# Kernel optimization log

Measured on AMD Instinct MI355X. Metric: run time of the kernel, lower is better.

The kernel has to match this reference:

```python
import jax, jax.numpy as jnp
import numpy as np

V, E, H = 50000, 256, 256   # vocab, emb_dim, hid_dim
R, S, W = 64, 32, 64        # reviews, sentences/review, words/sentence
UF = 20                     # user feature dim


def _bigru_last(x, wih, whh, bih, bhh):
    """Bidirectional GRU over x [B,T,D]; returns sum of final hidden states of
    the two directions, shape [B,H]. Params stacked over direction axis 0."""
    Hh = whh.shape[-1]

    def onedir(xd, wi, wh, bi, bh):
        gx = jnp.einsum('btd,gd->btg', xd, wi) + bi  # [B,T,3H] input gates precomputed

        def step(h, gxt):
            gh = h @ wh.T + bh
            r = jax.nn.sigmoid(gxt[:, :Hh] + gh[:, :Hh])
            z = jax.nn.sigmoid(gxt[:, Hh:2 * Hh] + gh[:, Hh:2 * Hh])
            n = jnp.tanh(gxt[:, 2 * Hh:] + r * gh[:, 2 * Hh:])
            return (1.0 - z) * n + z * h, None

        h0 = jnp.zeros((xd.shape[0], Hh), xd.dtype)
        hT, _ = jax.lax.scan(step, h0, jnp.swapaxes(gx, 0, 1))
        return hT

    return (onedir(x, wih[0], whh[0], bih[0], bhh[0])
            + onedir(x[:, ::-1], wih[1], whh[1], bih[1], bhh[1]))


def setup_inputs() -> dict:
    key = jax.random.key(0)
    ks = iter(jax.random.split(key, 40))

    def wmat(shape, scale=0.05):
        return jax.random.normal(next(ks), shape, jnp.float32) * scale

    inp = {}
    inp['inputs'] = jax.random.randint(next(ks), (R, S, W), 0, V)
    inp['sent_lengths'] = jax.random.randint(next(ks), (R, S), 1, W)
    inp['sent_counts'] = jax.random.randint(next(ks), (R,), 1, S)
    inp['user_feats'] = jax.random.normal(next(ks), (R, UF), jnp.float32)
    inp['embed'] = wmat((V, E))
    for name, din in (('wg', E), ('sg', H), ('rg', H + UF)):
        inp[name + '_wih'] = wmat((2, 3 * H, din))
        inp[name + '_whh'] = wmat((2, 3 * H, H))
        inp[name + '_bih'] = jnp.zeros((2, 3 * H), jnp.float32)
        inp[name + '_bhh'] = jnp.zeros((2, 3 * H), jnp.float32)
    inp['rfc_w1'] = wmat((H // 2, H + UF)); inp['rfc_b1'] = jnp.zeros((H // 2,), jnp.float32)
    inp['rfc_w2'] = wmat((1, H // 2));      inp['rfc_b2'] = jnp.zeros((1,), jnp.float32)
    inp['pfc_w1'] = wmat((H // 2, H));      inp['pfc_b1'] = jnp.zeros((H // 2,), jnp.float32)
    inp['pfc_w2'] = wmat((9, H // 2));      inp['pfc_b2'] = jnp.zeros((9,), jnp.float32)
    inp['uf_w'] = jnp.ones((UF,), jnp.float32)  # user_feats_weights
    return inp


def reference(inputs, sent_lengths, sent_counts, user_feats, embed,
              wg_wih, wg_whh, wg_bih, wg_bhh,
              sg_wih, sg_whh, sg_bih, sg_bhh,
              rg_wih, rg_whh, rg_bih, rg_bhh,
              rfc_w1, rfc_b1, rfc_w2, rfc_b2,
              pfc_w1, pfc_b1, pfc_w2, pfc_b2, uf_w):
    Rr, Sr, Wr = inputs.shape
    emb = embed[inputs]  # [R,S,W,E]  (dropout = identity in eval mode)
    # word-level bi-GRU, all R*S sentences batched together
    sent = _bigru_last(emb.reshape(Rr * Sr, Wr, emb.shape[-1]),
                       wg_wih, wg_whh, wg_bih, wg_bhh).reshape(Rr, Sr, -1)
    # sentence-level bi-GRU, batch over reviews
    rev = _bigru_last(sent, sg_wih, sg_whh, sg_bih, sg_bhh)  # [R,H]
    # F.normalize(user_feats) * user_feats_weights
    nrm = jnp.maximum(jnp.linalg.norm(user_feats, axis=-1, keepdims=True), 1e-12)
    p_batch = jnp.concatenate([rev, (user_feats / nrm) * uf_w], axis=-1)  # [R,H+20]
    r_stars = (jax.nn.selu(p_batch @ rfc_w1.T + rfc_b1) @ rfc_w2.T + rfc_b2)[:, 0]  # [R]
    # review-level bi-GRU over the sequence of reviews (batch 1)
    doc = _bigru_last(p_batch[None], rg_wih, rg_whh, rg_bih, rg_bhh)[0]  # [H]
    p_stars = jax.nn.selu(doc @ pfc_w1.T + pfc_b1) @ pfc_w2.T + pfc_b2  # [9]
    return p_stars, r_stars
```

## Files before the change

kernel.cpp:

```cpp
#include <hip/hip_runtime.h>
#include <math.h>

#define R_ 64
#define S_ 32
#define W_ 64
#define H_ 256
#define UF_ 20
#define TC 4

typedef short bf16x8 __attribute__((ext_vector_type(8)));
typedef float f32x4  __attribute__((ext_vector_type(4)));

#define MFMA(a,b,c) __builtin_amdgcn_mfma_f32_16x16x32_bf16((a),(b),(c),0,0,0)

__device__ __forceinline__ float sigf(float x){ return 1.0f/(1.0f+__expf(-x)); }
__device__ __forceinline__ float tanhf_(float x){ float e=__expf(2.0f*x); return 1.0f-2.0f/(e+1.0f); }
__device__ __forceinline__ float seluf_(float x){
  const float sc=1.0507009873554805f, al=1.6732632423543772f;
  return x>0.0f ? sc*x : sc*al*(expf(x)-1.0f);
}
__device__ __forceinline__ short tobf(float f){
  unsigned u=__float_as_uint(f); u += 0x7fffu + ((u>>16)&1u); return (short)(u>>16);
}
__device__ __forceinline__ float bf2f(short s){
  return __uint_as_float(((unsigned)(unsigned short)s) << 16);
}
__device__ __forceinline__ unsigned pk2(float a, float b){
  return (unsigned)(unsigned short)tobf(a) | ((unsigned)(unsigned short)tobf(b) << 16);
}

__global__ void prep_word_w(const float* __restrict__ wih, const float* __restrict__ whh,
                            short* __restrict__ Bw)
{
  int idx = blockIdx.x*256 + threadIdx.x;
  int lane = idx & 63;
  int rest = idx >> 6;
  int f  = rest % 6;  rest /= 6;
  int kt = rest % 16; rest /= 16;
  int w  = rest % 8;
  int d  = rest / 8;
  int gate = f >> 1;
  int j = 32*w + (f&1)*16 + (lane&15);
  int row = gate*256 + j;
  const float* W = (kt < 8 ? wih : whh) + (size_t)d*768*256;
  int k = (kt&7)*32 + (lane>>4)*8;
  short* dst = Bw + ((((size_t)(d*8 + w)*16 + kt)*6 + f)*64 + lane)*8;
#pragma unroll
  for (int jj=0;jj<8;jj++) dst[jj] = tobf(W[(size_t)row*256 + k + jj]);
}

__global__ void prep_rnn_w(const float* __restrict__ whh, short* __restrict__ Bs)
{
  int idx = blockIdx.x*256 + threadIdx.x;
  int lane = idx & 63;
  int rest = idx >> 6;
  int f  = rest % 6; rest /= 6;
  int kt = rest % 8; rest /= 8;
  int w  = rest % 8;
  int d  = rest / 8;
  int j = 32*w + (f&1)*16 + (lane&15);
  int row = (f>>1)*256 + j;
  const float* W = whh + (size_t)d*768*256;
  int k = kt*32 + (lane>>4)*8;
  short* dst = Bs + ((((size_t)(d*8 + w)*8 + kt)*6 + f)*64 + lane)*8;
#pragma unroll
  for (int jj=0;jj<8;jj++) dst[jj] = tobf(W[(size_t)row*256 + k + jj]);
}

__global__ void prep_gemm_w(const float* __restrict__ Wsrc, short* __restrict__ Bg)
{
  int idx = blockIdx.x*256 + threadIdx.x;
  int lane = idx & 63;
  int rest = idx >> 6;
  int kt = rest % 8;
  int nt = rest / 8;
  int n = nt*16 + (lane&15);
  int k = kt*32 + (lane>>4)*8;
  short* dst = Bg + (((size_t)nt*8 + kt)*64 + lane)*8;
#pragma unroll
  for (int jj=0;jj<8;jj++) dst[jj] = tobf(Wsrc[(size_t)n*256 + k + jj]);
}

__global__ __launch_bounds__(256) void gemm_gxu(
    const short* __restrict__ Ab, const float* __restrict__ Af,
    const int* __restrict__ toks, const short* __restrict__ Bg,
    short* __restrict__ C, long Czoff,
    int mode, int t0, int Mclamp, int Cstride)
{
  const int z  = blockIdx.z;
  const int m0 = blockIdx.x * 64;
  const int yt = blockIdx.y * 8;
  const int ntb = (mode == 2 ? z*48 : 0) + yt;
  const int tid = threadIdx.x;
  const int w = tid >> 6, l = tid & 63;
  const int c = l & 15, q = l >> 4;
  __shared__ short As[64][264];
  {
    const int row = tid >> 2, c0 = (tid & 3) * 64;
    if (mode == 0) {
      const uint4* s = (const uint4*)(Ab + (size_t)(m0+row)*256 + c0);
#pragma unroll
      for (int i = 0; i < 8; i++) *(uint4*)&As[row][c0 + i*8] = s[i];
    } else {
      int r;
      if (mode == 1) {
        r = m0 + row; if (r >= Mclamp) r = Mclamp - 1;
      } else {
        const int rr = m0 + row;
        const int s_ = rr / TC, i_ = rr % TC;
        const int wd = z ? (63 - (t0 + i_)) : (t0 + i_);
        r = toks[s_*64 + wd];
      }
      const float* s = Af + (size_t)r*256 + c0;
#pragma unroll
      for (int i = 0; i < 8; i++) {
        float4 v0 = *(const float4*)(s + i*8);
        float4 v1 = *(const float4*)(s + i*8 + 4);
        uint4 u;
        u.x = pk2(v0.x, v0.y); u.y = pk2(v0.z, v0.w);
        u.z = pk2(v1.x, v1.y); u.w = pk2(v1.z, v1.w);
        *(uint4*)&As[row][c0 + i*8] = u;
      }
    }
  }
  __syncthreads();
  f32x4 acc[4][2];
#pragma unroll
  for (int a = 0; a < 4; a++) { acc[a][0] = (f32x4)0.f; acc[a][1] = (f32x4)0.f; }
#pragma unroll
  for (int kt = 0; kt < 8; kt++) {
    const int ko = kt*32 + q*8;
    bf16x8 a0 = *(const bf16x8*)&As[ 0+c][ko];
    bf16x8 a1 = *(const bf16x8*)&As[16+c][ko];
    bf16x8 a2 = *(const bf16x8*)&As[32+c][ko];
    bf16x8 a3 = *(const bf16x8*)&As[48+c][ko];
    bf16x8 b0 = *(const bf16x8*)&Bg[(((size_t)(ntb + 2*w    )*8 + kt)*64 + l)*8];
    bf16x8 b1 = *(const bf16x8*)&Bg[(((size_t)(ntb + 2*w + 1)*8 + kt)*64 + l)*8];
    acc[0][0]=MFMA(a0,b0,acc[0][0]); acc[1][0]=MFMA(a1,b0,acc[1][0]);
    acc[2][0]=MFMA(a2,b0,acc[2][0]); acc[3][0]=MFMA(a3,b0,acc[3][0]);
    acc[0][1]=MFMA(a0,b1,acc[0][1]); acc[1][1]=MFMA(a1,b1,acc[1][1]);
    acc[2][1]=MFMA(a2,b1,acc[2][1]); acc[3][1]=MFMA(a3,b1,acc[3][1]);
  }
  short* Cz = C + (size_t)z * Czoff;
#pragma unroll
  for (int mt = 0; mt < 4; mt++)
#pragma unroll
  for (int nt = 0; nt < 2; nt++)
#pragma unroll
  for (int rg = 0; rg < 4; rg++)
    Cz[(size_t)(m0 + mt*16 + q*4 + rg)*Cstride + (yt + 2*w + nt)*16 + c] =
        tobf(acc[mt][nt][rg]);
}

__global__ __launch_bounds__(512, 2) void gru_rec(
    const int* __restrict__ toks,
    const short* __restrict__ gxF, const short* __restrict__ gxB,
    const short* __restrict__ Bh, int wstride, int koff,
    const float* __restrict__ bih, const float* __restrict__ bhh,
    float* __restrict__ hstate, int NS,
    int t0, int nsteps, int mode, int nwords)
{
  const int d = blockIdx.x & 1;
  const int g = blockIdx.x >> 1;
  const int tid = threadIdx.x;
  const int w = tid >> 6, l = tid & 63;
  const int c = l & 15, q = l >> 4;

  __shared__ short gbuf[2][16][784];
  __shared__ short hbf[2][16][264];
  __shared__ int   tokL[1024];

  if (mode == 0)
    for (int i = tid; i < 1024; i += 512) tokL[i] = toks[(size_t)g*1024 + i];

  bf16x8 Breg[8][6];
  {
    const short* Bb = Bh + (size_t)(d*8 + w)*wstride + (size_t)koff*3072 + l*8;
#pragma unroll
    for (int kt = 0; kt < 8; kt++)
#pragma unroll
    for (int f = 0; f < 6; f++)
      Breg[kt][f] = *(const bf16x8*)(Bb + (kt*6 + f)*512);
  }

  float bR[2], bZ[2], bNX[2], bNH[2];
#pragma unroll
  for (int jt = 0; jt < 2; jt++) {
    int j = 32*w + jt*16 + c;
    bR[jt]  = bih[d*768 + j]       + bhh[d*768 + j];
    bZ[jt]  = bih[d*768 + 256 + j] + bhh[d*768 + 256 + j];
    bNX[jt] = bih[d*768 + 512 + j];
    bNH[jt] = bhh[d*768 + 512 + j];
  }

  float hst[2][4];
  const int cur0 = t0 & 1;
  if (t0 == 0) {
#pragma unroll
    for (int a = 0; a < 2; a++)
#pragma unroll
    for (int r = 0; r < 4; r++) hst[a][r] = 0.0f;
  } else {
#pragma unroll
    for (int jt = 0; jt < 2; jt++)
#pragma unroll
    for (int rg = 0; rg < 4; rg++)
      hst[jt][rg] = hstate[((size_t)d*NS + g*16 + q*4 + rg)*256 + 32*w + jt*16 + c];
  }
#pragma unroll
  for (int jt = 0; jt < 2; jt++)
#pragma unroll
  for (int rg = 0; rg < 4; rg++)
    hbf[cur0][q*4 + rg][32*w + jt*16 + c] = tobf(hst[jt][rg]);

  __syncthreads();

  const int grow = tid >> 5;
  const int gcol = (tid & 31) * 24;

  for (int t = t0; t < t0 + nsteps; t++) {
    const int cur = t & 1, nxt = 1 - cur;
    {
      const short* src;
      if (mode == 0) {
        const int tx = d ? (nwords - 1 - t) : t;
        src = gxF + (size_t)tokL[grow*64 + tx]*1536 + d*768 + gcol;
      } else if (mode == 1) {
        const int r = (g*16 + grow)*TC + (t - t0);
        src = (d ? gxB : gxF) + (size_t)r*768 + gcol;
      } else {
        const int se = d ? (nwords - 1 - t) : t;
        src = gxF + ((size_t)(g*16 + grow)*nwords + se)*1536 + d*768 + gcol;
      }
      const uint4* s4 = (const uint4*)src;
      uint4 v0 = s4[0], v1 = s4[1], v2 = s4[2];
      uint4* dst = (uint4*)&gbuf[cur][grow][gcol];
      dst[0] = v0; dst[1] = v1; dst[2] = v2;
    }
    __syncthreads();

    f32x4 accR[2], accZ[2], accNH[2];
#pragma unroll
    for (int a = 0; a < 2; a++) { accR[a]=(f32x4)0.f; accZ[a]=(f32x4)0.f; accNH[a]=(f32x4)0.f; }
#pragma unroll
    for (int kt = 0; kt < 8; kt++) {
      bf16x8 a0 = *(const bf16x8*)&hbf[cur][c][kt*32 + q*8];
      accR[0]=MFMA(a0,Breg[kt][0],accR[0]);  accR[1]=MFMA(a0,Breg[kt][1],accR[1]);
      accZ[0]=MFMA(a0,Breg[kt][2],accZ[0]);  accZ[1]=MFMA(a0,Breg[kt][3],accZ[1]);
      accNH[0]=MFMA(a0,Breg[kt][4],accNH[0]); accNH[1]=MFMA(a0,Breg[kt][5],accNH[1]);
    }

#pragma unroll
    for (int jt = 0; jt < 2; jt++)
#pragma unroll
    for (int rg = 0; rg < 4; rg++) {
      const int m = q*4 + rg;
      const int j = 32*w + jt*16 + c;
      const float gr = bf2f(gbuf[cur][m][j]);
      const float gz = bf2f(gbuf[cur][m][256 + j]);
      const float gn = bf2f(gbuf[cur][m][512 + j]);
      const float r = sigf(gr + bR[jt] + accR[jt][rg]);
      const float z = sigf(gz + bZ[jt] + accZ[jt][rg]);
      const float n = tanhf_(gn + bNX[jt] + r*(accNH[jt][rg] + bNH[jt]));
      float h = hst[jt][rg];
      h = (1.0f - z)*n + z*h;
      hst[jt][rg] = h;
      hbf[nxt][m][j] = tobf(h);
    }
  }

#pragma unroll
  for (int jt = 0; jt < 2; jt++)
#pragma unroll
  for (int rg = 0; rg < 4; rg++)
    hstate[((size_t)d*NS + g*16 + q*4 + rg)*256 + 32*w + jt*16 + c] = hst[jt][rg];
}

__global__ void add2bf(const float* __restrict__ a, const float* __restrict__ b,
                       short* __restrict__ o)
{
  int i = (blockIdx.x*256 + threadIdx.x)*4;
  float4 x = *(const float4*)&a[i];
  float4 y = *(const float4*)&b[i];
  *(uint2*)&o[i] = make_uint2(pk2(x.x+y.x, x.y+y.y), pk2(x.z+y.z, x.w+y.w));
}

__global__ __launch_bounds__(512, 2) void rev_gru(
    const float* __restrict__ gx, const short* __restrict__ Br,
    const float* __restrict__ bih, const float* __restrict__ bhh,
    float* __restrict__ doc)
{
  const int d = blockIdx.x;
  const int tid = threadIdx.x;
  const int w = tid >> 6, l = tid & 63;
  const int c = l & 15, q = l >> 4;

  __shared__ short hbf[16][264];
  for (int i = tid; i < 16*264; i += 512) ((short*)hbf)[i] = 0;

  bf16x8 Breg[8][6];
  {
    const short* Bbase = Br + (size_t)(d*8 + w)*8*6*512 + l*8;
#pragma unroll
    for (int kt = 0; kt < 8; kt++)
#pragma unroll
    for (int f = 0; f < 6; f++)
      Breg[kt][f] = *(const bf16x8*)(Bbase + (kt*6 + f)*512);
  }

  float bR[2], bZ[2], bNX[2], bNH[2];
#pragma unroll
  for (int jt = 0; jt < 2; jt++) {
    int j = 32*w + jt*16 + c;
    bR[jt]  = bih[d*768 + j]       + bhh[d*768 + j];
    bZ[jt]  = bih[d*768 + 256 + j] + bhh[d*768 + 256 + j];
    bNX[jt] = bih[d*768 + 512 + j];
    bNH[jt] = bhh[d*768 + 512 + j];
  }
  float hst[2][4];
#pragma unroll
  for (int a=0;a<2;a++)
#pragma unroll
  for (int r=0;r<4;r++) hst[a][r] = 0.0f;
  __syncthreads();

  for (int t = 0; t < 64; t++) {
    const int teff = (d == 0) ? t : (63 - t);
    float gr[2], gz[2], gn[2];
#pragma unroll
    for (int jt = 0; jt < 2; jt++) {
      const int j = 32*w + jt*16 + c;
      const size_t row = (size_t)teff*1536 + d*768;
      gr[jt] = gx[row + j]; gz[jt] = gx[row + 256 + j]; gn[jt] = gx[row + 512 + j];
    }
    f32x4 accR[2], accZ[2], accNH[2];
#pragma unroll
    for (int a=0;a<2;a++) { accR[a]=(f32x4)0.f; accZ[a]=(f32x4)0.f; accNH[a]=(f32x4)0.f; }
#pragma unroll
    for (int kt = 0; kt < 8; kt++) {
      bf16x8 a0 = *(const bf16x8*)&hbf[c][kt*32 + q*8];
      accR[0]=MFMA(a0,Breg[kt][0],accR[0]);  accR[1]=MFMA(a0,Breg[kt][1],accR[1]);
      accZ[0]=MFMA(a0,Breg[kt][2],accZ[0]);  accZ[1]=MFMA(a0,Breg[kt][3],accZ[1]);
      accNH[0]=MFMA(a0,Breg[kt][4],accNH[0]); accNH[1]=MFMA(a0,Breg[kt][5],accNH[1]);
    }
    __syncthreads();
#pragma unroll
    for (int jt = 0; jt < 2; jt++)
#pragma unroll
    for (int rg = 0; rg < 4; rg++) {
      const float r = sigf(gr[jt] + bR[jt] + accR[jt][rg]);
      const float z = sigf(gz[jt] + bZ[jt] + accZ[jt][rg]);
      const float n = tanhf_(gn[jt] + bNX[jt] + r*(accNH[jt][rg] + bNH[jt]));
      float h = hst[jt][rg];
      h = (1.0f - z)*n + z*h;
      hst[jt][rg] = h;
      hbf[q*4 + rg][32*w + jt*16 + c] = tobf(h);
    }
    __syncthreads();
  }
  if (q == 0) {
#pragma unroll
    for (int jt = 0; jt < 2; jt++)
      doc[d*256 + 32*w + jt*16 + c] = hst[jt][0];
  }
}

__global__ __launch_bounds__(256) void gemm_nt16(
    const float* __restrict__ A, const float* __restrict__ B, float* __restrict__ C,
    int M, int N, int K)
{
  const int m0 = blockIdx.x * 16;
  const int n0 = blockIdx.y * 64;
  const int tid = threadIdx.x;
  __shared__ float As[16][17];
  __shared__ float Bs[16][68];
  float acc[4] = {0,0,0,0};
  const int m  = tid >> 4, n4 = (tid & 15) * 4;
  const int bn = tid >> 2, bk = (tid & 3) * 4;
  for (int k0 = 0; k0 < K; k0 += 16) {
    const int ak = tid & 15;
    float av = (k0 + ak < K) ? A[(size_t)(m0+m)*K + k0 + ak] : 0.0f;
    float4 b4 = make_float4(0,0,0,0);
    if (k0 + bk < K) b4 = *(const float4*)&B[(size_t)(n0+bn)*K + k0 + bk];
    __syncthreads();
    As[ak][m] = av;
    Bs[bk+0][bn]=b4.x; Bs[bk+1][bn]=b4.y; Bs[bk+2][bn]=b4.z; Bs[bk+3][bn]=b4.w;
    __syncthreads();
#pragma unroll
    for (int k = 0; k < 16; k++) {
      const float a = As[k][m];
      const float4 bb = *(const float4*)&Bs[k][n4];
      acc[0]+=a*bb.x; acc[1]+=a*bb.y; acc[2]+=a*bb.z; acc[3]+=a*bb.w;
    }
  }
  *(float4*)&C[(size_t)(m0+m)*N + n0+n4] = make_float4(acc[0],acc[1],acc[2],acc[3]);
}

__global__ void pbatch_k(const float* __restrict__ hs, const float* __restrict__ uf,
                         const float* __restrict__ ufw, float* __restrict__ pb)
{
  const int r = blockIdx.x, tid = threadIdx.x;
  __shared__ float nrm;
  if (tid == 0) {
    float s = 0.f;
    for (int i = 0; i < UF_; i++) { const float v = uf[r*UF_ + i]; s += v*v; }
    nrm = fmaxf(sqrtf(s), 1e-12f);
  }
  __syncthreads();
  if (tid < H_)  pb[r*276 + tid] = hs[r*H_ + tid] + hs[(size_t)R_*H_ + r*H_ + tid];
  if (tid < UF_) pb[r*276 + H_ + tid] = uf[r*UF_ + tid] / nrm * ufw[tid];
}

__global__ void rstars_k(const float* __restrict__ pb,
                         const float* __restrict__ w1, const float* __restrict__ b1,
                         const float* __restrict__ w2, const float* __restrict__ b2,
                         float* __restrict__ out)
{
  const int r = blockIdx.x, tid = threadIdx.x;
  __shared__ float ps[276];
  __shared__ float s1[128];
  for (int i = tid; i < 276; i += 128) ps[i] = pb[r*276 + i];
  __syncthreads();
  float a = b1[tid];
  for (int k = 0; k < 276; k++) a += ps[k] * w1[tid*276 + k];
  s1[tid] = seluf_(a);
  __syncthreads();
  if (tid == 0) {
    float s = b2[0];
    for (int k = 0; k < 128; k++) s += s1[k] * w2[k];
    out[9 + r] = s;
  }
}

__global__ void pstars_k(const float* __restrict__ doc2,
                         const float* __restrict__ w1, const float* __restrict__ b1,
                         const float* __restrict__ w2, const float* __restrict__ b2,
                         float* __restrict__ out)
{
  const int tid = threadIdx.x;
  __shared__ float dc[256];
  __shared__ float s1[128];
  dc[tid]       = doc2[tid]       + doc2[256 + tid];
  dc[128 + tid] = doc2[128 + tid] + doc2[384 + tid];
  __syncthreads();
  float a = b1[tid];
  for (int k = 0; k < 256; k++) a += dc[k] * w1[tid*256 + k];
  s1[tid] = seluf_(a);
  __syncthreads();
  if (tid < 9) {
    float s = b2[tid];
    for (int k = 0; k < 128; k++) s += s1[k] * w2[tid*128 + k];
    out[tid] = s;
  }
}

extern "C" void kernel_launch(void* const* d_in, const int* in_sizes, int n_in,
                              void* d_out, int out_size, void* d_ws, size_t ws_size,
                              hipStream_t stream)
{
  const int*   toks   = (const int*)  d_in[0];
  const float* uf     = (const float*)d_in[3];
  const float* embed  = (const float*)d_in[4];
  const float* wg_wih = (const float*)d_in[5];
  const float* wg_whh = (const float*)d_in[6];
  const float* wg_bih = (const float*)d_in[7];
  const float* wg_bhh = (const float*)d_in[8];
  const float* sg_wih = (const float*)d_in[9];
  const float* sg_whh = (const float*)d_in[10];
  const float* sg_bih = (const float*)d_in[11];
  const float* sg_bhh = (const float*)d_in[12];
  const float* rg_wih = (const float*)d_in[13];
  const float* rg_whh = (const float*)d_in[14];
  const float* rg_bih = (const float*)d_in[15];
  const float* rg_bhh = (const float*)d_in[16];
  const float* rfc_w1 = (const float*)d_in[17];
  const float* rfc_b1 = (const float*)d_in[18];
  const float* rfc_w2 = (const float*)d_in[19];
  const float* rfc_b2 = (const float*)d_in[20];
  const float* pfc_w1 = (const float*)d_in[21];
  const float* pfc_b1 = (const float*)d_in[22];
  const float* pfc_w2 = (const float*)d_in[23];
  const float* pfc_b2 = (const float*)d_in[24];
  const float* uf_w   = (const float*)d_in[25];
  float* out = (float*)d_out;
  float* ws  = (float*)d_ws;
  (void)in_sizes; (void)n_in; (void)out_size;

  const size_t OFF_BW   = 0;
  const size_t OFF_BS   = OFF_BW  + 393216;
  const size_t OFF_BR   = OFF_BS  + 196608;
  const size_t OFF_BG   = OFF_BR  + 196608;
  const size_t OFF_BGW  = OFF_BG  + 196608;
  const size_t OFF_HF   = OFF_BGW + 196608;
  const size_t OFF_SB   = OFF_HF  + 1048576;
  const size_t OFF_GXS  = OFF_SB  + 262144;
  const size_t OFF_HS   = OFF_GXS + 1572864;
  const size_t OFF_PB   = OFF_HS  + 32768;
  const size_t OFF_GXR  = OFF_PB  + 17664;
  const size_t OFF_DOC  = OFF_GXR + 98304;
  const size_t OFF_GXT  = OFF_DOC + 512;
  const size_t TOT_A    = OFF_GXT + (size_t)50048*1536/2;

  short* Bw   = (short*)(ws + OFF_BW);
  short* Bs   = (short*)(ws + OFF_BS);
  short* Br   = (short*)(ws + OFF_BR);
  short* Bg   = (short*)(ws + OFF_BG);
  short* Bgw  = (short*)(ws + OFF_BGW);
  float* hfin = ws + OFF_HF;
  short* sentb= (short*)(ws + OFF_SB);
  short* gxs  = (short*)(ws + OFF_GXS);
  float* hs   = ws + OFF_HS;
  float* pb   = ws + OFF_PB;
  float* gxr  = ws + OFF_GXR;
  float* doc  = ws + OFF_DOC;
  short* gxf  = (short*)(ws + OFF_GXT);
  short* gxb  = gxf + (size_t)8192*768;
  short* gxv  = (short*)(ws + OFF_GXT);

  const bool big = ws_size >= TOT_A * sizeof(float);

  prep_word_w<<<384, 256, 0, stream>>>(wg_wih, wg_whh, Bw);
  prep_rnn_w<<<192, 256, 0, stream>>>(sg_whh, Bs);
  prep_rnn_w<<<192, 256, 0, stream>>>(rg_whh, Br);
  prep_gemm_w<<<192, 256, 0, stream>>>(sg_wih, Bg);
  prep_gemm_w<<<192, 256, 0, stream>>>(wg_wih, Bgw);

  if (big) {
    gemm_gxu<<<dim3(782, 12, 1), 256, 0, stream>>>(
        nullptr, embed, nullptr, Bgw, gxv, 0, 1, 0, 50000, 1536);
    gru_rec<<<256, 512, 0, stream>>>(toks, gxv, nullptr, Bw, 49152, 8,
        wg_bih, wg_bhh, hfin, 2048, 0, 64, 0, 64);
  } else {
    for (int tc = 0; tc < 64/TC; tc++) {
      gemm_gxu<<<dim3(128, 6, 2), 256, 0, stream>>>(
          nullptr, embed, toks, Bgw, gxf, (long)8192*768, 2, tc*TC, 0, 768);
      gru_rec<<<256, 512, 0, stream>>>(toks, gxf, gxb, Bw, 49152, 8,
          wg_bih, wg_bhh, hfin, 2048, tc*TC, TC, 1, 64);
    }
  }
  add2bf<<<512, 256, 0, stream>>>(hfin, hfin + (size_t)2048*256, sentb);

  gemm_gxu<<<dim3(32, 12, 1), 256, 0, stream>>>(
      sentb, nullptr, nullptr, Bg, gxs, 0, 0, 0, 2048, 1536);
  gru_rec<<<8, 512, 0, stream>>>(nullptr, gxs, nullptr, Bs, 24576, 0,
      sg_bih, sg_bhh, hs, 64, 0, 32, 2, 32);

  pbatch_k<<<R_, 256, 0, stream>>>(hs, uf, uf_w, pb);
  rstars_k<<<R_, 128, 0, stream>>>(pb, rfc_w1, rfc_b1, rfc_w2, rfc_b2, out);

  gemm_nt16<<<dim3(4, 24), 256, 0, stream>>>(pb, rg_wih, gxr, 64, 1536, 276);
  rev_gru<<<2, 512, 0, stream>>>(gxr, Br, rg_bih, rg_bhh, doc);
  pstars_k<<<1, 128, 0, stream>>>(doc, pfc_w1, pfc_b1, pfc_w2, pfc_b2, out);
}
```

Baseline: 803.4 us.

## Prefetch gate inputs async into LDS and split recurrent weights registers/LDS

The recurrent GRU kernel now issues global_load_lds copies of the next step's precomputed input gates while the current step computes, removing one barrier per step and the register round-trip of the gate staging. Recurrent weight fragments are split so 40 of 48 stay in registers and 8 live in LDS, cutting VGPR pressure. The review-level GRU switches to a double-buffered hidden state to drop a barrier per step. The cost is extra LDS traffic for weight fragments, plus a dependence on correct ordering of the async LDS loads relative to the single remaining barrier.

```diff
diff --git a/kernel.cpp b/kernel.cpp
--- a/kernel.cpp
+++ b/kernel.cpp
@@ -12,6 +12,14 @@
 typedef float f32x4  __attribute__((ext_vector_type(4)));
 
 #define MFMA(a,b,c) __builtin_amdgcn_mfma_f32_16x16x32_bf16((a),(b),(c),0,0,0)
+
+typedef const unsigned int __attribute__((address_space(1)))* gp_t;
+typedef unsigned int __attribute__((address_space(3)))* lp_t;
+#define GLOAD16(SRC, DST) \
+  __builtin_amdgcn_global_load_lds((gp_t)(const void*)(SRC), (lp_t)(void*)(DST), 16, 0, 0)
+
+#define BFRAG(ff) ((ff) < 40 ? Breg[(ff) < 40 ? (ff) : 0] \
+                 : *(const bf16x8*)&Bl[w][(ff) >= 40 ? (ff)-40 : 0][l*8])
 
 __device__ __forceinline__ float sigf(float x){ return 1.0f/(1.0f+__expf(-x)); }
 __device__ __forceinline__ float tanhf_(float x){ float e=__expf(2.0f*x); return 1.0f-2.0f/(e+1.0f); }
@@ -152,6 +160,36 @@
         tobf(acc[mt][nt][rg]);
 }
 
+__device__ __forceinline__ void stage_issue(
+    short* dstbase,
+    int mode, int d, int g, int w, int l,
+    int nwords, int t0, int tt,
+    const int* tokp, const short* gxF, const short* gxB)
+{
+  const char* bF = (const char*)gxF;
+  const char* bB = (const char*)gxB;
+#pragma unroll
+  for (int i = 0; i < 3; i++) {
+    const int off = i*1024 + l*16;
+    const int rl  = (off >= 1536) ? 1 : 0;
+    const int col = off - rl*1536;
+    const char* src;
+    if (mode == 0) {
+      const int tx  = d ? (nwords - 1 - tt) : tt;
+      const int tok = tokp[(2*w + rl)*64 + tx];
+      src = bF + (size_t)tok*3072 + d*1536 + col;
+    } else if (mode == 1) {
+      const int ri = (g*16 + 2*w + rl)*TC + (tt - t0);
+      src = (d ? bB : bF) + (size_t)ri*1536 + col;
+    } else {
+      const int se  = d ? (nwords - 1 - tt) : tt;
+      const int row = g*16 + 2*w + rl;
+      src = bF + ((size_t)row*nwords + se)*3072 + (size_t)d*1536 + col;
+    }
+    GLOAD16(src, dstbase + (size_t)w*1536 + i*512);
+  }
+}
+
 __global__ __launch_bounds__(512, 2) void gru_rec(
     const int* __restrict__ toks,
     const short* __restrict__ gxF, const short* __restrict__ gxB,
@@ -166,21 +204,23 @@
   const int w = tid >> 6, l = tid & 63;
   const int c = l & 15, q = l >> 4;
 
-  __shared__ short gbuf[2][16][784];
+  __shared__ short gbuf[2][16][768];
   __shared__ short hbf[2][16][264];
+  __shared__ short Bl[8][8][512];
   __shared__ int   tokL[1024];
 
   if (mode == 0)
     for (int i = tid; i < 1024; i += 512) tokL[i] = toks[(size_t)g*1024 + i];
 
-  bf16x8 Breg[8][6];
+  bf16x8 Breg[40];
   {
     const short* Bb = Bh + (size_t)(d*8 + w)*wstride + (size_t)koff*3072 + l*8;
 #pragma unroll
-    for (int kt = 0; kt < 8; kt++)
-#pragma unroll
-    for (int f = 0; f < 6; f++)
-      Breg[kt][f] = *(const bf16x8*)(Bb + (kt*6 + f)*512);
+    for (int ff = 0; ff < 48; ff++) {
+      bf16x8 v = *(const bf16x8*)(Bb + ff*512);
+      if (ff < 40) Breg[ff] = v;
+      else *(bf16x8*)&Bl[w][ff-40][l*8] = v;
+    }
   }
 
   float bR[2], bZ[2], bNX[2], bNH[2];
@@ -213,31 +253,18 @@
   for (int rg = 0; rg < 4; rg++)
     hbf[cur0][q*4 + rg][32*w + jt*16 + c] = tobf(hst[jt][rg]);
 
-  __syncthreads();
-
-  const int grow = tid >> 5;
-  const int gcol = (tid & 31) * 24;
-
-  for (int t = t0; t < t0 + nsteps; t++) {
+  stage_issue((short*)gbuf[cur0], mode, d, g, w, l, nwords, t0, t0,
+              (mode == 0) ? toks + (size_t)g*1024 : (const int*)nullptr, gxF, gxB);
+
+  __syncthreads();
+
+  const int tend = t0 + nsteps;
+  for (int t = t0; t < tend; t++) {
     const int cur = t & 1, nxt = 1 - cur;
-    {
-      const short* src;
-      if (mode == 0) {
-        const int tx = d ? (nwords - 1 - t) : t;
-        src = gxF + (size_t)tokL[grow*64 + tx]*1536 + d*768 + gcol;
-      } else if (mode == 1) {
-        const int r = (g*16 + grow)*TC + (t - t0);
-        src = (d ? gxB : gxF) + (size_t)r*768 + gcol;
-      } else {
-        const int se = d ? (nwords - 1 - t) : t;
-        src = gxF + ((size_t)(g*16 + grow)*nwords + se)*1536 + d*768 + gcol;
-      }
-      const uint4* s4 = (const uint4*)src;
-      uint4 v0 = s4[0], v1 = s4[1], v2 = s4[2];
-      uint4* dst = (uint4*)&gbuf[cur][grow][gcol];
-      dst[0] = v0; dst[1] = v1; dst[2] = v2;
-    }
-    __syncthreads();
+
+    if (t + 1 < tend)
+      stage_issue((short*)gbuf[nxt], mode, d, g, w, l, nwords, t0, t + 1,
+                  tokL, gxF, gxB);
 
     f32x4 accR[2], accZ[2], accNH[2];
 #pragma unroll
@@ -245,9 +272,11 @@
 #pragma unroll
     for (int kt = 0; kt < 8; kt++) {
       bf16x8 a0 = *(const bf16x8*)&hbf[cur][c][kt*32 + q*8];
-      accR[0]=MFMA(a0,Breg[kt][0],accR[0]);  accR[1]=MFMA(a0,Breg[kt][1],accR[1]);
-      accZ[0]=MFMA(a0,Breg[kt][2],accZ[0]);  accZ[1]=MFMA(a0,Breg[kt][3],accZ[1]);
-      accNH[0]=MFMA(a0,Breg[kt][4],accNH[0]); accNH[1]=MFMA(a0,Breg[kt][5],accNH[1]);
+      bf16x8 b0 = BFRAG(kt*6+0), b1 = BFRAG(kt*6+1), b2 = BFRAG(kt*6+2),
+             b3 = BFRAG(kt*6+3), b4 = BFRAG(kt*6+4), b5 = BFRAG(kt*6+5);
+      accR[0]=MFMA(a0,b0,accR[0]);  accR[1]=MFMA(a0,b1,accR[1]);
+      accZ[0]=MFMA(a0,b2,accZ[0]);  accZ[1]=MFMA(a0,b3,accZ[1]);
+      accNH[0]=MFMA(a0,b4,accNH[0]); accNH[1]=MFMA(a0,b5,accNH[1]);
     }
 
 #pragma unroll
@@ -267,6 +296,7 @@
       hst[jt][rg] = h;
       hbf[nxt][m][j] = tobf(h);
     }
+    __syncthreads();
   }
 
 #pragma unroll
@@ -295,17 +325,19 @@
   const int w = tid >> 6, l = tid & 63;
   const int c = l & 15, q = l >> 4;
 
-  __shared__ short hbf[16][264];
-  for (int i = tid; i < 16*264; i += 512) ((short*)hbf)[i] = 0;
-
-  bf16x8 Breg[8][6];
+  __shared__ short hbf[2][16][264];
+  __shared__ short Bl[8][8][512];
+  for (int i = tid; i < 16*264; i += 512) ((short*)hbf[0])[i] = 0;
+
+  bf16x8 Breg[40];
   {
     const short* Bbase = Br + (size_t)(d*8 + w)*8*6*512 + l*8;
 #pragma unroll
-    for (int kt = 0; kt < 8; kt++)
-#pragma unroll
-    for (int f = 0; f < 6; f++)
-      Breg[kt][f] = *(const bf16x8*)(Bbase + (kt*6 + f)*512);
+    for (int ff = 0; ff < 48; ff++) {
+      bf16x8 v = *(const bf16x8*)(Bbase + ff*512);
+      if (ff < 40) Breg[ff] = v;
+      else *(bf16x8*)&Bl[w][ff-40][l*8] = v;
+    }
   }
 
   float bR[2], bZ[2], bNX[2], bNH[2];
@@ -325,6 +357,7 @@
   __syncthreads();
 
   for (int t = 0; t < 64; t++) {
+    const int cur = t & 1, nxt = 1 - cur;
     const int teff = (d == 0) ? t : (63 - t);
     float gr[2], gz[2], gn[2];
 #pragma unroll
@@ -338,12 +371,13 @@
     for (int a=0;a<2;a++) { accR[a]=(f32x4)0.f; accZ[a]=(f32x4)0.f; accNH[a]=(f32x4)0.f; }
 #pragma unroll
     for (int kt = 0; kt < 8; kt++) {
-      bf16x8 a0 = *(const bf16x8*)&hbf[c][kt*32 + q*8];
-      accR[0]=MFMA(a0,Breg[kt][0],accR[0]);  accR[1]=MFMA(a0,Breg[kt][1],accR[1]);
-      accZ[0]=MFMA(a0,Breg[kt][2],accZ[0]);  accZ[1]=MFMA(a0,Breg[kt][3],accZ[1]);
-      accNH[0]=MFMA(a0,Breg[kt][4],accNH[0]); accNH[1]=MFMA(a0,Breg[kt][5],accNH[1]);
-    }
-    __syncthreads();
+      bf16x8 a0 = *(const bf16x8*)&hbf[cur][c][kt*32 + q*8];
+      bf16x8 b0 = BFRAG(kt*6+0), b1 = BFRAG(kt*6+1), b2 = BFRAG(kt*6+2),
+             b3 = BFRAG(kt*6+3), b4 = BFRAG(kt*6+4), b5 = BFRAG(kt*6+5);
+      accR[0]=MFMA(a0,b0,accR[0]);  accR[1]=MFMA(a0,b1,accR[1]);
+      accZ[0]=MFMA(a0,b2,accZ[0]);  accZ[1]=MFMA(a0,b3,accZ[1]);
+      accNH[0]=MFMA(a0,b4,accNH[0]); accNH[1]=MFMA(a0,b5,accNH[1]);
+    }
 #pragma unroll
     for (int jt = 0; jt < 2; jt++)
 #pragma unroll
@@ -354,7 +388,7 @@
       float h = hst[jt][rg];
       h = (1.0f - z)*n + z*h;
       hst[jt][rg] = h;
-      hbf[q*4 + rg][32*w + jt*16 + c] = tobf(h);
+      hbf[nxt][q*4 + rg][32*w + jt*16 + c] = tobf(h);
     }
     __syncthreads();
   }
```

After: 783.9 us. -2.4%, faster.
